# Performance work log

Hardware: AMD Instinct MI355X
Metric: run time of the kernel (lower is better)

## Reference

```python
import jax, jax.numpy as jnp
import numpy as np

CAP = 15.0
EPS = 1e-6
NUM_HEADS = 16
HEAD_DIM = 64

def _rmsnorm(x, w):
    xf = x.astype(jnp.float32)
    var = jnp.mean(xf * xf, axis=-1, keepdims=True)
    return w * (xf * jax.lax.rsqrt(var + EPS)).astype(x.dtype)

def _gate(g):
    # sigmoid(soft_cap(g)) with cap 15
    return jax.nn.sigmoid(CAP * jnp.tanh(g / CAP))

def setup_inputs() -> dict:
    key = jax.random.key(0)
    ks = jax.random.split(key, 4)
    B, S, D = 4, 2048, 1024
    H, Dh = NUM_HEADS, HEAD_DIM
    return {
        "x": jax.random.normal(ks[0], (B, S, D), jnp.float32),
        "hidden_state": jnp.zeros((B, H, Dh, Dh), jnp.float32),
        "w_rms": jnp.ones((D,), jnp.float32),
        "w_qkv": jax.random.normal(ks[1], (D, 3 * H * Dh), jnp.float32) * 0.02,
        "w_gate": jax.random.normal(ks[2], (D, 3 * H), jnp.float32) * 0.02,
        "w_out": jax.random.normal(ks[3], (D, D), jnp.float32) * 0.02,
    }

def reference(x, hidden_state, w_rms, w_qkv, w_gate, w_out):
    B, S, D = x.shape
    H, Dh = NUM_HEADS, HEAD_DIM
    residual = x
    xn = _rmsnorm(x, w_rms)
    qkv = (xn @ w_qkv).reshape(B, S, 3, H, Dh)
    q, k, v = qkv[:, :, 0], qkv[:, :, 1], qkv[:, :, 2]  # [B,S,H,Dh]
    gates = _gate((xn @ w_gate).reshape(B, S, 3, H))
    i_g, f_g, o_g = gates[:, :, 0], gates[:, :, 1], gates[:, :, 2]  # [B,S,H]

    # time-major for scan: [S,B,H,...]
    def tm(a):
        return jnp.moveaxis(a, 1, 0)

    def step(state, inp):
        qt, kt, vt, it, ft, ot = inp  # [B,H,Dh]/[B,H]
        kv = kt[..., :, None] * vt[..., None, :]            # [B,H,Dh,Dh]
        state = ft[..., None, None] * state + it[..., None, None] * kv
        h = jnp.einsum('bhd,bhde->bhe', qt, state) * ot[..., None]
        return state, h

    _, h_seq = jax.lax.scan(step, hidden_state,
                            (tm(q), tm(k), tm(v), tm(i_g), tm(f_g), tm(o_g)))
    out = jnp.moveaxis(h_seq, 0, 1).reshape(B, S, H * Dh) @ w_out
    return residual + out
```

## Files before the change

### kernel.cpp

```cpp
#include <hip/hip_runtime.h>
#include <math.h>

typedef unsigned short u16;
typedef unsigned int   u32;
typedef __bf16 bf16x8 __attribute__((ext_vector_type(8)));
typedef float  f32x4  __attribute__((ext_vector_type(4)));

#define NBATCH 4
#define SEQ    2048
#define DIM    1024
#define NH     16
#define BH     64
#define NC     32
#define ROWS   8192
#define N1     3200

__device__ __forceinline__ u16 f2bf(float f) {
  u32 u = __builtin_bit_cast(u32, f);
  u32 r = u + 0x7fffu + ((u >> 16) & 1u);
  return (u16)(r >> 16);
}
__device__ __forceinline__ float bf2f(u16 h) {
  return __builtin_bit_cast(float, (u32)h << 16);
}

__device__ __forceinline__ void gl2lds16(const u16* g, u16* l) {
  __builtin_amdgcn_global_load_lds(
      (const __attribute__((address_space(1))) u32*)g,
      (__attribute__((address_space(3))) u32*)l, 16, 0, 0);
}

__global__ __launch_bounds__(256) void transpose_w(const float* __restrict__ W,
                                                   u16* __restrict__ Bt, int K, int N) {
  __shared__ float tile[32][33];
  const int n0 = blockIdx.x * 32, k0 = blockIdx.y * 32;
  const int tx = threadIdx.x, ty = threadIdx.y;
  #pragma unroll
  for (int i = 0; i < 4; i++)
    tile[ty + i * 8][tx] = W[(size_t)(k0 + ty + i * 8) * N + n0 + tx];
  __syncthreads();
  #pragma unroll
  for (int i = 0; i < 4; i++)
    Bt[(size_t)(n0 + ty + i * 8) * K + k0 + tx] = f2bf(tile[tx][ty + i * 8]);
}

__global__ __launch_bounds__(256) void fill_gateW(const float* __restrict__ wg,
                                                  u16* __restrict__ Bt) {
  const int g = blockIdx.x;
  const int tid = threadIdx.x;
  #pragma unroll
  for (int kk = 0; kk < 4; kk++) {
    const int k = kk * 256 + tid;
    u16 v = 0;
    if (g < 48) v = f2bf(wg[(size_t)k * 48 + g]);
    Bt[(size_t)(3072 + g) * 1024 + k] = v;
  }
}

__global__ __launch_bounds__(256) void rmsnorm_k(const float* __restrict__ x,
                                                 const float* __restrict__ w,
                                                 u16* __restrict__ xn) {
  const int row = blockIdx.x, tid = threadIdx.x;
  const float4 xv = *(const float4*)&x[(size_t)row * 1024 + tid * 4];
  float ss = xv.x * xv.x + xv.y * xv.y + xv.z * xv.z + xv.w * xv.w;
  #pragma unroll
  for (int off = 32; off > 0; off >>= 1) ss += __shfl_down(ss, off);
  __shared__ float red[4];
  if ((tid & 63) == 0) red[tid >> 6] = ss;
  __syncthreads();
  const float tot = red[0] + red[1] + red[2] + red[3];
  const float scale = rsqrtf(tot * (1.0f / 1024.0f) + 1e-6f);
  const float4 wv = *(const float4*)&w[tid * 4];
  const u16 o0 = f2bf(xv.x * scale * wv.x), o1 = f2bf(xv.y * scale * wv.y);
  const u16 o2 = f2bf(xv.z * scale * wv.z), o3 = f2bf(xv.w * scale * wv.w);
  uint2 ov;
  ov.x = (u32)o0 | ((u32)o1 << 16);
  ov.y = (u32)o2 | ((u32)o3 << 16);
  *(uint2*)&xn[(size_t)row * 1024 + tid * 4] = ov;
}

__device__ __forceinline__ void gemm_core256(const u16* __restrict__ A, const u16* __restrict__ Bt,
                                             int K, int rowBase, int colBase,
                                             u16* As, u16* Bs, f32x4 (&acc)[4][4]) {
  const int tid = threadIdx.x;
  const int lane = tid & 63;
  const int q = lane >> 4, m16 = lane & 15;
  const int wave = tid >> 6;
  const int wm = wave & 3, wn = wave >> 2;
  const u16* gA[4]; u16* lA[4];
  const u16* gB[2]; u16* lB[2];
  #pragma unroll
  for (int j = 0; j < 4; j++) {
    const int c = tid + j * 512;
    const int half = c >> 10, cc = c & 1023;
    gA[j] = &A[(size_t)(rowBase + (cc >> 2)) * K + half * 32 + (cc & 3) * 8];
    lA[j] = As + c * 8;
  }
  #pragma unroll
  for (int j = 0; j < 2; j++) {
    const int c = tid + j * 512;
    const int half = c >> 9, cc = c & 511;
    gB[j] = &Bt[(size_t)(colBase + (cc >> 2)) * K + half * 32 + (cc & 3) * 8];
    lB[j] = Bs + c * 8;
  }
  for (int kb = 0; kb < K / 64; ++kb) {
    __syncthreads();
    #pragma unroll
    for (int j = 0; j < 4; j++) { gl2lds16(gA[j], lA[j]); gA[j] += 64; }
    #pragma unroll
    for (int j = 0; j < 2; j++) { gl2lds16(gB[j], lB[j]); gB[j] += 64; }
    __syncthreads();
    #pragma unroll
    for (int ks = 0; ks < 2; ks++) {
      const int aoff = ks * 8192;
      const int boff = ks * 4096;
      bf16x8 af[4], bfr[4];
      #pragma unroll
      for (int mi = 0; mi < 4; mi++)
        af[mi] = *(const bf16x8*)&As[aoff + (wm * 64 + mi * 16 + m16) * 32 + q * 8];
      #pragma unroll
      for (int ni = 0; ni < 4; ni++)
        bfr[ni] = *(const bf16x8*)&Bs[boff + (wn * 64 + ni * 16 + m16) * 32 + q * 8];
      #pragma unroll
      for (int mi = 0; mi < 4; mi++)
        #pragma unroll
        for (int ni = 0; ni < 4; ni++)
          acc[mi][ni] = __builtin_amdgcn_mfma_f32_16x16x32_bf16(af[mi], bfr[ni], acc[mi][ni], 0, 0, 0);
    }
  }
}

__device__ __forceinline__ void gemm_core128(const u16* __restrict__ A, const u16* __restrict__ Bt,
                                             int K, int rowBase, int colBase,
                                             u16* As, u16* Bs, f32x4 (&acc)[4][4]) {
  const int tid = threadIdx.x;
  const int lane = tid & 63;
  const int q = lane >> 4, m16 = lane & 15;
  const int wave = tid >> 6;
  const int wm = wave & 1, wn = wave >> 1;
  const u16* gA[4]; u16* lA[4];
  const u16* gB[4]; u16* lB[4];
  #pragma unroll
  for (int j = 0; j < 4; j++) {
    const int c = tid + j * 256;
    const int half = c >> 9, cc = c & 511;
    gA[j] = &A [(size_t)(rowBase + (cc >> 2)) * K + half * 32 + (cc & 3) * 8];
    lA[j] = As + c * 8;
    gB[j] = &Bt[(size_t)(colBase + (cc >> 2)) * K + half * 32 + (cc & 3) * 8];
    lB[j] = Bs + c * 8;
  }
  for (int kb = 0; kb < K / 64; ++kb) {
    __syncthreads();
    #pragma unroll
    for (int j = 0; j < 4; j++) { gl2lds16(gA[j], lA[j]); gA[j] += 64; }
    #pragma unroll
    for (int j = 0; j < 4; j++) { gl2lds16(gB[j], lB[j]); gB[j] += 64; }
    __syncthreads();
    #pragma unroll
    for (int ks = 0; ks < 2; ks++) {
      const int off = ks * 4096;
      bf16x8 af[4], bfr[4];
      #pragma unroll
      for (int mi = 0; mi < 4; mi++)
        af[mi] = *(const bf16x8*)&As[off + (wm * 64 + mi * 16 + m16) * 32 + q * 8];
      #pragma unroll
      for (int ni = 0; ni < 4; ni++)
        bfr[ni] = *(const bf16x8*)&Bs[off + (wn * 64 + ni * 16 + m16) * 32 + q * 8];
      #pragma unroll
      for (int mi = 0; mi < 4; mi++)
        #pragma unroll
        for (int ni = 0; ni < 4; ni++)
          acc[mi][ni] = __builtin_amdgcn_mfma_f32_16x16x32_bf16(af[mi], bfr[ni], acc[mi][ni], 0, 0, 0);
    }
  }
}

__global__ __launch_bounds__(512, 4) void gemm_qkv(const u16* __restrict__ A, const u16* __restrict__ Bt,
                                                   u16* __restrict__ Qb, u16* __restrict__ Kb,
                                                   u16* __restrict__ Vb, float* __restrict__ gates) {
  __shared__ __attribute__((aligned(16))) u16 As[256 * 64];
  __shared__ __attribute__((aligned(16))) u16 Bs[128 * 64];
  f32x4 acc[4][4] = {};
  const int rowBase = blockIdx.x * 256, colBase = blockIdx.y * 128;
  gemm_core256(A, Bt, 1024, rowBase, colBase, As, Bs, acc);
  const int tid = threadIdx.x;
  const int lane = tid & 63, wave = tid >> 6;
  const int q = lane >> 4, m16 = lane & 15;
  const int wm = wave & 3, wn = wave >> 2;
  __syncthreads();
  if (colBase < 3072) {
    const int which = colBase >> 10;
    u16* dstBase = (which == 0) ? Qb : ((which == 1) ? Kb : Vb);
    const int b = rowBase >> 11;
    const int h = ((colBase & 1023) >> 6) + wn;
    const int tRow0 = (rowBase & 2047) + wm * 64;
    u16* scratch = As + wave * 1024;
    u16* headBase = dstBase + ((size_t)(b * 16 + h)) * 2048 * 64;
    const int rr = lane >> 2, co = (lane & 3) * 16;
    #pragma unroll
    for (int mi = 0; mi < 4; mi++) {
      #pragma unroll
      for (int ni = 0; ni < 4; ni++)
        #pragma unroll
        for (int r = 0; r < 4; r++)
          scratch[(q * 4 + r) * 64 + ni * 16 + m16] = f2bf(acc[mi][ni][r]);
      const uint4 d0 = *(const uint4*)&scratch[rr * 64 + co];
      const uint4 d1 = *(const uint4*)&scratch[rr * 64 + co + 8];
      u16* gp = headBase + (size_t)(tRow0 + mi * 16 + rr) * 64 + co;
      *(uint4*)gp = d0;
      *(uint4*)(gp + 8) = d1;
    }
  } else {
    #pragma unroll
    for (int ni = 0; ni < 4; ni++) {
      const int c2 = wn * 64 + ni * 16 + m16;
      if (c2 < 48) {
        const int which = c2 >> 4, hh = c2 & 15;
        #pragma unroll
        for (int mi = 0; mi < 4; mi++)
          #pragma unroll
          for (int r = 0; r < 4; r++) {
            const int grow = rowBase + wm * 64 + mi * 16 + q * 4 + r;
            const int b = grow >> 11, t = grow & 2047;
            const float v = acc[mi][ni][r];
            const float g = 1.0f / (1.0f + expf(-(15.0f * tanhf(v * (1.0f / 15.0f)))));
            gates[((size_t)which * 64 + (b * 16 + hh)) * 2048 + t] = g;
          }
      }
    }
  }
}

__global__ __launch_bounds__(256, 4) void gemm_out(const u16* __restrict__ A, const u16* __restrict__ Bt,
                                                   const float* __restrict__ resid,
                                                   float* __restrict__ out) {
  __shared__ __attribute__((aligned(16))) u16 As[128 * 64];
  __shared__ __attribute__((aligned(16))) u16 Bs[128 * 64];
  f32x4 acc[4][4] = {};
  const int rowBase = blockIdx.x * 128, colBase = blockIdx.y * 128;
  gemm_core128(A, Bt, 1024, rowBase, colBase, As, Bs, acc);
  const int tid = threadIdx.x;
  const int lane = tid & 63, wave = tid >> 6;
  const int q = lane >> 4, m16 = lane & 15;
  const int wm = wave & 1, wn = wave >> 1;
  #pragma unroll
  for (int mi = 0; mi < 4; mi++)
    #pragma unroll
    for (int ni = 0; ni < 4; ni++)
      #pragma unroll
      for (int r = 0; r < 4; r++) {
        const int grow = rowBase + wm * 64 + mi * 16 + q * 4 + r;
        const int gcol = colBase + wn * 64 + ni * 16 + m16;
        const size_t idx = (size_t)grow * 1024 + gcol;
        out[idx] = acc[mi][ni][r] + resid[idx];
      }
}

__global__ __launch_bounds__(256) void passA_k(const u16* __restrict__ Qb, const u16* __restrict__ Kb,
                                               const u16* __restrict__ Vb,
                                               const float* __restrict__ gates,
                                               float* __restrict__ la,
                                               u16* __restrict__ Mbuf, u16* __restrict__ hseq) {
  __shared__ u16 Ql[64][72], Kl[64][72], KTl[64][72], VTl[64][72], Pl[64][72];
  __shared__ float laS[64], iS[64];
  const int tid = threadIdx.x;
  const int bh = blockIdx.x >> 5, c = blockIdx.x & 31;
  const int lane = tid & 63, w = tid >> 6;
  const int q = lane >> 4, m16 = lane & 15;
  const size_t base = ((size_t)bh * 2048 + c * 64) * 64;
  const int toff = c * 64;

  if (tid < 64) {
    float lg = logf(gates[(size_t)(64 + bh) * 2048 + toff + tid]);
    #pragma unroll
    for (int off = 1; off < 64; off <<= 1) {
      const float y = __shfl_up(lg, off);
      if (tid >= off) lg += y;
    }
    laS[tid] = lg;
    iS[tid] = gates[(size_t)bh * 2048 + toff + tid];
    la[(size_t)bh * 2048 + toff + tid] = lg;
  }
  __syncthreads();

  {
    const int s = tid >> 2, db = (tid & 3) * 16;
    const float wk = expf(laS[63] - laS[s]) * iS[s];
    const uint4 q0 = *(const uint4*)&Qb[base + s * 64 + db];
    const uint4 q1 = *(const uint4*)&Qb[base + s * 64 + db + 8];
    *(uint4*)&Ql[s][db] = q0;
    *(uint4*)&Ql[s][db + 8] = q1;
    const uint4 k0 = *(const uint4*)&Kb[base + s * 64 + db];
    const uint4 k1 = *(const uint4*)&Kb[base + s * 64 + db + 8];
    *(uint4*)&Kl[s][db] = k0;
    *(uint4*)&Kl[s][db + 8] = k1;
    u16 ktmp[16];
    *(uint4*)&ktmp[0] = k0;
    *(uint4*)&ktmp[8] = k1;
    #pragma unroll
    for (int j = 0; j < 16; j++) KTl[db + j][s] = f2bf(wk * bf2f(ktmp[j]));
    const uint4 v0 = *(const uint4*)&Vb[base + s * 64 + db];
    const uint4 v1 = *(const uint4*)&Vb[base + s * 64 + db + 8];
    u16 vtmp[16];
    *(uint4*)&vtmp[0] = v0;
    *(uint4*)&vtmp[8] = v1;
    #pragma unroll
    for (int j = 0; j < 16; j++) VTl[db + j][s] = vtmp[j];
  }
  __syncthreads();

  f32x4 pacc[4] = {};
  #pragma unroll
  for (int ks = 0; ks < 2; ks++) {
    const bf16x8 aq = *(const bf16x8*)&Ql[w * 16 + m16][ks * 32 + q * 8];
    #pragma unroll
    for (int ni = 0; ni < 4; ni++) {
      const bf16x8 bk = *(const bf16x8*)&Kl[ni * 16 + m16][ks * 32 + q * 8];
      pacc[ni] = __builtin_amdgcn_mfma_f32_16x16x32_bf16(aq, bk, pacc[ni], 0, 0, 0);
    }
  }
  #pragma unroll
  for (int ni = 0; ni < 4; ni++)
    #pragma unroll
    for (int r = 0; r < 4; r++) {
      const int tt = w * 16 + q * 4 + r, ss = ni * 16 + m16;
      float Wts = 0.0f;
      if (ss <= tt) Wts = expf(laS[tt] - laS[ss]) * iS[ss];
      Pl[tt][ss] = f2bf(pacc[ni][r] * Wts);
    }
  __syncthreads();

  f32x4 hacc[4] = {}, macc[4] = {};
  #pragma unroll
  for (int ks = 0; ks < 2; ks++) {
    const bf16x8 ap = *(const bf16x8*)&Pl[w * 16 + m16][ks * 32 + q * 8];
    const bf16x8 av = *(const bf16x8*)&VTl[w * 16 + m16][ks * 32 + q * 8];
    #pragma unroll
    for (int ni = 0; ni < 4; ni++) {
      const bf16x8 bv = *(const bf16x8*)&VTl[ni * 16 + m16][ks * 32 + q * 8];
      const bf16x8 bk = *(const bf16x8*)&KTl[ni * 16 + m16][ks * 32 + q * 8];
      hacc[ni] = __builtin_amdgcn_mfma_f32_16x16x32_bf16(ap, bv, hacc[ni], 0, 0, 0);
      macc[ni] = __builtin_amdgcn_mfma_f32_16x16x32_bf16(av, bk, macc[ni], 0, 0, 0);
    }
  }
  const int b = bh >> 4, h = bh & 15;
  #pragma unroll
  for (int ni = 0; ni < 4; ni++)
    #pragma unroll
    for (int r = 0; r < 4; r++) {
      const int tt = w * 16 + q * 4 + r, e = ni * 16 + m16;
      const int tg = c * 64 + tt;
      hseq[((size_t)b * 2048 + tg) * 1024 + h * 64 + e] = f2bf(hacc[ni][r]);
      Mbuf[(((size_t)bh * 32 + c) * 64 + tt) * 64 + e] = f2bf(macc[ni][r]);
    }
}

__global__ __launch_bounds__(256) void passB_k(u16* __restrict__ Mbuf,
                                               const float* __restrict__ hidden,
                                               const float* __restrict__ la) {
  const int bh = blockIdx.x >> 4;
  const int e = (blockIdx.x & 15) * 256 + threadIdx.x;
  __shared__ float Gs[32];
  if (threadIdx.x < 32)
    Gs[threadIdx.x] = expf(la[(size_t)bh * 2048 + threadIdx.x * 64 + 63]);
  __syncthreads();
  const int eRow = e >> 6, dCol = e & 63;
  float st = hidden[(size_t)bh * 4096 + dCol * 64 + eRow];
  u16* M = &Mbuf[(size_t)bh * 32 * 4096 + e];
  float m_next = bf2f(M[0]);
  #pragma unroll 4
  for (int c = 0; c < 32; c++) {
    const float m_cur = m_next;
    if (c < 31) m_next = bf2f(M[(size_t)(c + 1) * 4096]);
    M[(size_t)c * 4096] = f2bf(st);
    st = Gs[c] * st + m_cur;
  }
}

__global__ __launch_bounds__(256) void passC_k(const u16* __restrict__ Qb,
                                               const u16* __restrict__ SprevT,
                                               const float* __restrict__ la,
                                               const float* __restrict__ gates,
                                               u16* __restrict__ hseq) {
  __shared__ u16 aQl[64][72], STl[64][72];
  __shared__ float laS[64], oS[64];
  const int tid = threadIdx.x;
  const int bh = blockIdx.x >> 5, c = blockIdx.x & 31;
  const int lane = tid & 63, w = tid >> 6;
  const int q = lane >> 4, m16 = lane & 15;
  const size_t base = ((size_t)bh * 2048 + c * 64) * 64;
  const int toff = c * 64;
  if (tid < 64) {
    laS[tid] = la[(size_t)bh * 2048 + toff + tid];
    oS[tid] = gates[(size_t)(128 + bh) * 2048 + toff + tid];
  }
  {
    const int s = tid >> 2, db = (tid & 3) * 16;
    *(uint4*)&aQl[s][db]     = *(const uint4*)&Qb[base + s * 64 + db];
    *(uint4*)&aQl[s][db + 8] = *(const uint4*)&Qb[base + s * 64 + db + 8];
    const u16* SpT = &SprevT[((size_t)bh * 32 + c) * 4096];
    *(uint4*)&STl[s][db]     = *(const uint4*)&SpT[s * 64 + db];
    *(uint4*)&STl[s][db + 8] = *(const uint4*)&SpT[s * 64 + db + 8];
  }
  __syncthreads();
  f32x4 acc[4] = {};
  #pragma unroll
  for (int ks = 0; ks < 2; ks++) {
    const bf16x8 a = *(const bf16x8*)&aQl[w * 16 + m16][ks * 32 + q * 8];
    #pragma unroll
    for (int ni = 0; ni < 4; ni++) {
      const bf16x8 bb = *(const bf16x8*)&STl[ni * 16 + m16][ks * 32 + q * 8];
      acc[ni] = __builtin_amdgcn_mfma_f32_16x16x32_bf16(a, bb, acc[ni], 0, 0, 0);
    }
  }
  const int b = bh >> 4, h = bh & 15;
  #pragma unroll
  for (int ni = 0; ni < 4; ni++)
    #pragma unroll
    for (int r = 0; r < 4; r++) {
      const int tt = w * 16 + q * 4 + r, e = ni * 16 + m16;
      const int tg = c * 64 + tt;
      const float a_t = expf(laS[tt]);
      const float o = oS[tt];
      const size_t idx = ((size_t)b * 2048 + tg) * 1024 + h * 64 + e;
      hseq[idx] = f2bf(o * (bf2f(hseq[idx]) + a_t * acc[ni][r]));
    }
}

extern "C" void kernel_launch(void* const* d_in, const int* in_sizes, int n_in,
                              void* d_out, int out_size, void* d_ws, size_t ws_size,
                              hipStream_t stream) {
  (void)in_sizes; (void)n_in; (void)out_size; (void)ws_size;
  const float* x      = (const float*)d_in[0];
  const float* hidden = (const float*)d_in[1];
  const float* w_rms  = (const float*)d_in[2];
  const float* w_qkv  = (const float*)d_in[3];
  const float* w_gate = (const float*)d_in[4];
  const float* w_out  = (const float*)d_in[5];
  float* out = (float*)d_out;

  char* p = (char*)d_ws;
  u16* wqkvT = (u16*)p;  p += (size_t)N1 * 1024 * 2;
  u16* woutT = (u16*)p;  p += (size_t)1024 * 1024 * 2;
  u16* xn    = (u16*)p;  p += (size_t)ROWS * 1024 * 2;
  u16* Qb    = (u16*)p;  p += (size_t)BH * 2048 * 64 * 2;
  u16* Kb    = (u16*)p;  p += (size_t)BH * 2048 * 64 * 2;
  u16* Vb    = (u16*)p;  p += (size_t)BH * 2048 * 64 * 2;
  float* gates = (float*)p; p += (size_t)3 * BH * 2048 * 4;
  float* la    = (float*)p; p += (size_t)BH * 2048 * 4;
  u16* Mbuf  = (u16*)p;  p += (size_t)BH * NC * 4096 * 2;
  u16* hseq  = (u16*)p;  p += (size_t)ROWS * 1024 * 2;

  transpose_w<<<dim3(96, 32), dim3(32, 8), 0, stream>>>(w_qkv, wqkvT, 1024, 3072);
  transpose_w<<<dim3(32, 32), dim3(32, 8), 0, stream>>>(w_out, woutT, 1024, 1024);
  fill_gateW<<<128, 256, 0, stream>>>(w_gate, wqkvT);
  rmsnorm_k<<<ROWS, 256, 0, stream>>>(x, w_rms, xn);
  gemm_qkv<<<dim3(32, 25), 512, 0, stream>>>(xn, wqkvT, Qb, Kb, Vb, gates);
  passA_k<<<BH * NC, 256, 0, stream>>>(Qb, Kb, Vb, gates, la, Mbuf, hseq);
  passB_k<<<BH * 16, 256, 0, stream>>>(Mbuf, hidden, la);
  passC_k<<<BH * NC, 256, 0, stream>>>(Qb, Mbuf, la, gates, hseq);
  gemm_out<<<dim3(64, 8), 256, 0, stream>>>(hseq, woutT, x, out);
}
```

Before: 264.5 us.

## Rewrite QKV GEMM as 256x256 double-buffered pipelined kernel with swizzled LDS

Replaces the QKV projection GEMM with a 256x256-tile kernel using a 128KB double-buffered LDS ring. Global-to-LDS loads for the next tile are interleaved with MFMA phases under explicit barriers, vmcnt waits and setprio. LDS columns are XOR-swizzled to avoid bank conflicts, and the block index is remapped for L2 locality. Padding the gate-weight columns to 3328 adds a small amount of wasted compute, and occupancy drops to two blocks per CU.

```diff
diff --git a/kernel.cpp b/kernel.cpp
--- a/kernel.cpp
+++ b/kernel.cpp
@@ -13,7 +13,7 @@
 #define BH     64
 #define NC     32
 #define ROWS   8192
-#define N1     3200
+#define N1     3328
 
 __device__ __forceinline__ u16 f2bf(float f) {
   u32 u = __builtin_bit_cast(u32, f);
@@ -79,53 +79,150 @@
   *(uint2*)&xn[(size_t)row * 1024 + tid * 4] = ov;
 }
 
-__device__ __forceinline__ void gemm_core256(const u16* __restrict__ A, const u16* __restrict__ Bt,
-                                             int K, int rowBase, int colBase,
-                                             u16* As, u16* Bs, f32x4 (&acc)[4][4]) {
+
+#define FENCE asm volatile("" ::: "memory")
+#define SBAR  do { FENCE; __builtin_amdgcn_s_barrier(); FENCE; } while (0)
+#define WAITV4 do { FENCE; asm volatile("s_waitcnt vmcnt(4)" ::: "memory"); } while (0)
+#define WAITV0 do { FENCE; asm volatile("s_waitcnt vmcnt(0)" ::: "memory"); } while (0)
+
+#define STAGE_A(BUF, HALF, TILE) do { \
+  const u16* s_ = Abase + (size_t)(TILE) * 64 + (size_t)(HALF) * 131072; \
+  u16* l_ = &lds[((BUF) * 4 + (HALF)) * 8192 + tid * 8]; \
+  gl2lds16(s_, l_); gl2lds16(s_ + 65536, l_ + 4096); \
+} while (0)
+
+#define STAGE_B(BUF, HALF, TILE) do { \
+  const u16* s_ = Bbase + (size_t)(TILE) * 64 + (size_t)(HALF) * 131072; \
+  u16* l_ = &lds[((BUF) * 4 + 2 + (HALF)) * 8192 + tid * 8]; \
+  gl2lds16(s_, l_); gl2lds16(s_ + 65536, l_ + 4096); \
+} while (0)
+
+#define READ_A(ALDS, MH) do { \
+  _Pragma("unroll") \
+  for (int mi_ = 0; mi_ < 4; ++mi_) { \
+    af[mi_][0] = *(const bf16x8*)((ALDS) + (MH) * 4096 + mi_ * 1024 + co0); \
+    af[mi_][1] = *(const bf16x8*)((ALDS) + (MH) * 4096 + mi_ * 1024 + co1); \
+  } \
+} while (0)
+
+#define READ_B(BLDS, NH) do { \
+  _Pragma("unroll") \
+  for (int ni_ = 0; ni_ < 2; ++ni_) { \
+    bfr[NH][ni_][0] = *(const bf16x8*)((BLDS) + (NH) * 2048 + ni_ * 1024 + co0); \
+    bfr[NH][ni_][1] = *(const bf16x8*)((BLDS) + (NH) * 2048 + ni_ * 1024 + co1); \
+  } \
+} while (0)
+
+#define MFMA16(MH, NH) do { \
+  __builtin_amdgcn_s_setprio(1); \
+  _Pragma("unroll") \
+  for (int mi_ = 0; mi_ < 4; ++mi_) { \
+    _Pragma("unroll") \
+    for (int ni_ = 0; ni_ < 2; ++ni_) { \
+      acc[(MH)*4+mi_][(NH)*2+ni_] = __builtin_amdgcn_mfma_f32_16x16x32_bf16( \
+          af[mi_][0], bfr[NH][ni_][0], acc[(MH)*4+mi_][(NH)*2+ni_], 0, 0, 0); \
+      acc[(MH)*4+mi_][(NH)*2+ni_] = __builtin_amdgcn_mfma_f32_16x16x32_bf16( \
+          af[mi_][1], bfr[NH][ni_][1], acc[(MH)*4+mi_][(NH)*2+ni_], 0, 0, 0); \
+    } \
+  } \
+  __builtin_amdgcn_s_setprio(0); \
+} while (0)
+
+#define GITER(T, FULL) do { \
+   READ_A(aLds0, 0); READ_B(bLds0, 0); STAGE_A(1, 0, 2*(T)+1); \
+         SBAR; MFMA16(0, 0); SBAR; \
+   READ_B(bLds0, 1); STAGE_A(1, 1, 2*(T)+1); \
+         SBAR; MFMA16(0, 1); SBAR; \
+   READ_A(aLds0, 1); if (FULL) STAGE_B(0, 0, 2*(T)+2); \
+         SBAR; MFMA16(1, 0); SBAR; \
+   if (FULL) STAGE_B(0, 1, 2*(T)+2); \
+         SBAR; MFMA16(1, 1); if (FULL) { WAITV4; } else { WAITV0; } SBAR; \
+   READ_A(aLds1, 0); READ_B(bLds1, 0); if (FULL) STAGE_A(0, 0, 2*(T)+2); \
+         SBAR; MFMA16(0, 0); SBAR; \
+   READ_B(bLds1, 1); if (FULL) STAGE_A(0, 1, 2*(T)+2); \
+         SBAR; MFMA16(0, 1); SBAR; \
+   READ_A(aLds1, 1); if (FULL) STAGE_B(1, 0, 2*(T)+3); \
+         SBAR; MFMA16(1, 0); SBAR; \
+   if (FULL) STAGE_B(1, 1, 2*(T)+3); \
+         SBAR; MFMA16(1, 1); if (FULL) { WAITV4; } SBAR; \
+} while (0)
+
+__global__ __launch_bounds__(512, 2) void gemm_qkv(const u16* __restrict__ A, const u16* __restrict__ Bt,
+                                                   u16* __restrict__ Qb, u16* __restrict__ Kb,
+                                                   u16* __restrict__ Vb, float* __restrict__ gates) {
+  __shared__ __attribute__((aligned(16))) u16 lds[65536];
   const int tid = threadIdx.x;
-  const int lane = tid & 63;
+  const int lane = tid & 63, wave = tid >> 6;
   const int q = lane >> 4, m16 = lane & 15;
-  const int wave = tid >> 6;
-  const int wm = wave & 3, wn = wave >> 2;
-  const u16* gA[4]; u16* lA[4];
-  const u16* gB[2]; u16* lB[2];
-  #pragma unroll
-  for (int j = 0; j < 4; j++) {
-    const int c = tid + j * 512;
-    const int half = c >> 10, cc = c & 1023;
-    gA[j] = &A[(size_t)(rowBase + (cc >> 2)) * K + half * 32 + (cc & 3) * 8];
-    lA[j] = As + c * 8;
-  }
-  #pragma unroll
-  for (int j = 0; j < 2; j++) {
-    const int c = tid + j * 512;
-    const int half = c >> 9, cc = c & 511;
-    gB[j] = &Bt[(size_t)(colBase + (cc >> 2)) * K + half * 32 + (cc & 3) * 8];
-    lB[j] = Bs + c * 8;
-  }
-  for (int kb = 0; kb < K / 64; ++kb) {
-    __syncthreads();
-    #pragma unroll
-    for (int j = 0; j < 4; j++) { gl2lds16(gA[j], lA[j]); gA[j] += 64; }
-    #pragma unroll
-    for (int j = 0; j < 2; j++) { gl2lds16(gB[j], lB[j]); gB[j] += 64; }
-    __syncthreads();
-    #pragma unroll
-    for (int ks = 0; ks < 2; ks++) {
-      const int aoff = ks * 8192;
-      const int boff = ks * 4096;
-      bf16x8 af[4], bfr[4];
+  const int wm = wave & 1, wn = wave >> 1;
+
+  const int g = blockIdx.x;
+  const int swz = (g & 7) * 52 + (g >> 3);
+  const int bm = swz & 31, bn = swz >> 5;
+  const int rowBase = bm * 256, colBase = bn * 256;
+
+  const int sx = m16 & 7;
+  const int co0 = (q ^ sx) * 8;
+  const int co1 = ((4 + q) ^ sx) * 8;
+
+  const int r0 = tid >> 3, pc = tid & 7;
+  const int lcg = pc ^ (r0 & 7);
+  const u16* Abase = A  + (size_t)rowBase * 1024 + (size_t)r0 * 1024 + lcg * 8;
+  const u16* Bbase = Bt + (size_t)colBase * 1024 + (size_t)r0 * 1024 + lcg * 8;
+
+  const u16* aLds0 = &lds[wm * 8192 + m16 * 64];
+  const u16* aLds1 = aLds0 + 32768;
+  const u16* bLds0 = &lds[16384 + (wn >> 1) * 8192 + ((wn & 1) * 64 + m16) * 64];
+  const u16* bLds1 = bLds0 + 32768;
+
+  bf16x8 af[4][2];
+  bf16x8 bfr[2][2][2];
+  f32x4 acc[8][4] = {};
+
+  STAGE_A(0, 0, 0); STAGE_A(0, 1, 0); STAGE_B(0, 0, 0); STAGE_B(0, 1, 0);
+  STAGE_B(1, 0, 1); STAGE_B(1, 1, 1);
+  WAITV4; SBAR;
+
+  #pragma unroll 1
+  for (int t = 0; t < 7; ++t) GITER(t, 1);
+  GITER(7, 0);
+
+  const int rr = lane >> 2, co = (lane & 3) * 16;
+  if (colBase < 3072) {
+    const int which = colBase >> 10;
+    u16* dstBase = (which == 0) ? Qb : ((which == 1) ? Kb : Vb);
+    const int b = rowBase >> 11;
+    const int h = ((colBase & 1023) >> 6) + wn;
+    const int tRow0 = (rowBase & 2047) + wm * 128;
+    u16* headBase = dstBase + ((size_t)(b * 16 + h)) * 2048 * 64;
+    u16* scratch = lds + wave * 1024;
+    #pragma unroll
+    for (int mi = 0; mi < 8; ++mi) {
       #pragma unroll
-      for (int mi = 0; mi < 4; mi++)
-        af[mi] = *(const bf16x8*)&As[aoff + (wm * 64 + mi * 16 + m16) * 32 + q * 8];
+      for (int bj = 0; bj < 4; ++bj)
+        #pragma unroll
+        for (int r = 0; r < 4; ++r)
+          scratch[(q * 4 + r) * 64 + bj * 16 + m16] = f2bf(acc[mi][bj][r]);
+      const uint4 d0 = *(const uint4*)&scratch[rr * 64 + co];
+      const uint4 d1 = *(const uint4*)&scratch[rr * 64 + co + 8];
+      u16* gp = headBase + (size_t)(tRow0 + mi * 16 + rr) * 64 + co;
+      *(uint4*)gp = d0;
+      *(uint4*)(gp + 8) = d1;
+    }
+  } else {
+    if (wn == 0) {
       #pragma unroll
-      for (int ni = 0; ni < 4; ni++)
-        bfr[ni] = *(const bf16x8*)&Bs[boff + (wn * 64 + ni * 16 + m16) * 32 + q * 8];
-      #pragma unroll
-      for (int mi = 0; mi < 4; mi++)
+      for (int ai = 0; ai < 8; ++ai)
         #pragma unroll
-        for (int ni = 0; ni < 4; ni++)
-          acc[mi][ni] = __builtin_amdgcn_mfma_f32_16x16x32_bf16(af[mi], bfr[ni], acc[mi][ni], 0, 0, 0);
+        for (int bj = 0; bj < 3; ++bj)
+          #pragma unroll
+          for (int r = 0; r < 4; ++r) {
+            const int grow = rowBase + wm * 128 + ai * 16 + q * 4 + r;
+            const int b = grow >> 11, tt = grow & 2047;
+            const float v = acc[ai][bj][r];
+            const float gg = 1.0f / (1.0f + expf(-(15.0f * tanhf(v * (1.0f / 15.0f)))));
+            gates[((size_t)bj * 64 + (b * 16 + m16)) * 2048 + tt] = gg;
+          }
     }
   }
 }
@@ -171,62 +268,6 @@
         #pragma unroll
         for (int ni = 0; ni < 4; ni++)
           acc[mi][ni] = __builtin_amdgcn_mfma_f32_16x16x32_bf16(af[mi], bfr[ni], acc[mi][ni], 0, 0, 0);
-    }
-  }
-}
-
-__global__ __launch_bounds__(512, 4) void gemm_qkv(const u16* __restrict__ A, const u16* __restrict__ Bt,
-                                                   u16* __restrict__ Qb, u16* __restrict__ Kb,
-                                                   u16* __restrict__ Vb, float* __restrict__ gates) {
-  __shared__ __attribute__((aligned(16))) u16 As[256 * 64];
-  __shared__ __attribute__((aligned(16))) u16 Bs[128 * 64];
-  f32x4 acc[4][4] = {};
-  const int rowBase = blockIdx.x * 256, colBase = blockIdx.y * 128;
-  gemm_core256(A, Bt, 1024, rowBase, colBase, As, Bs, acc);
-  const int tid = threadIdx.x;
-  const int lane = tid & 63, wave = tid >> 6;
-  const int q = lane >> 4, m16 = lane & 15;
-  const int wm = wave & 3, wn = wave >> 2;
-  __syncthreads();
-  if (colBase < 3072) {
-    const int which = colBase >> 10;
-    u16* dstBase = (which == 0) ? Qb : ((which == 1) ? Kb : Vb);
-    const int b = rowBase >> 11;
-    const int h = ((colBase & 1023) >> 6) + wn;
-    const int tRow0 = (rowBase & 2047) + wm * 64;
-    u16* scratch = As + wave * 1024;
-    u16* headBase = dstBase + ((size_t)(b * 16 + h)) * 2048 * 64;
-    const int rr = lane >> 2, co = (lane & 3) * 16;
-    #pragma unroll
-    for (int mi = 0; mi < 4; mi++) {
-      #pragma unroll
-      for (int ni = 0; ni < 4; ni++)
-        #pragma unroll
-        for (int r = 0; r < 4; r++)
-          scratch[(q * 4 + r) * 64 + ni * 16 + m16] = f2bf(acc[mi][ni][r]);
-      const uint4 d0 = *(const uint4*)&scratch[rr * 64 + co];
-      const uint4 d1 = *(const uint4*)&scratch[rr * 64 + co + 8];
-      u16* gp = headBase + (size_t)(tRow0 + mi * 16 + rr) * 64 + co;
-      *(uint4*)gp = d0;
-      *(uint4*)(gp + 8) = d1;
-    }
-  } else {
-    #pragma unroll
-    for (int ni = 0; ni < 4; ni++) {
-      const int c2 = wn * 64 + ni * 16 + m16;
-      if (c2 < 48) {
-        const int which = c2 >> 4, hh = c2 & 15;
-        #pragma unroll
-        for (int mi = 0; mi < 4; mi++)
-          #pragma unroll
-          for (int r = 0; r < 4; r++) {
-            const int grow = rowBase + wm * 64 + mi * 16 + q * 4 + r;
-            const int b = grow >> 11, t = grow & 2047;
-            const float v = acc[mi][ni][r];
-            const float g = 1.0f / (1.0f + expf(-(15.0f * tanhf(v * (1.0f / 15.0f)))));
-            gates[((size_t)which * 64 + (b * 16 + hh)) * 2048 + t] = g;
-          }
-      }
     }
   }
 }
@@ -453,9 +494,9 @@
 
   transpose_w<<<dim3(96, 32), dim3(32, 8), 0, stream>>>(w_qkv, wqkvT, 1024, 3072);
   transpose_w<<<dim3(32, 32), dim3(32, 8), 0, stream>>>(w_out, woutT, 1024, 1024);
-  fill_gateW<<<128, 256, 0, stream>>>(w_gate, wqkvT);
+  fill_gateW<<<256, 256, 0, stream>>>(w_gate, wqkvT);
   rmsnorm_k<<<ROWS, 256, 0, stream>>>(x, w_rms, xn);
-  gemm_qkv<<<dim3(32, 25), 512, 0, stream>>>(xn, wqkvT, Qb, Kb, Vb, gates);
+  gemm_qkv<<<416, 512, 0, stream>>>(xn, wqkvT, Qb, Kb, Vb, gates);
   passA_k<<<BH * NC, 256, 0, stream>>>(Qb, Kb, Vb, gates, la, Mbuf, hseq);
   passB_k<<<BH * 16, 256, 0, stream>>>(Mbuf, hidden, la);
   passC_k<<<BH * NC, 256, 0, stream>>>(Qb, Mbuf, la, gates, hseq);
```

After: 264.1 us. Within noise of the previous version (-0.2%).
